# Kernel optimization log

Hardware: AMD Instinct MI355X
Metric: run time of the kernel (lower is better)

## Reference

```python
import jax, jax.numpy as jnp
import numpy as np

HIDDEN = 1024
HEADS = 16
HEAD_DIM = HIDDEN // HEADS

def setup_inputs() -> dict:
    key = jax.random.key(0)
    k1, k2, k3 = jax.random.split(key, 3)
    scale = 1.0 / np.sqrt(HIDDEN)
    return {
        "x": jax.random.normal(k1, (2, 2048, HIDDEN), dtype=jnp.float32),
        "w_qkv": jax.random.normal(k2, (HIDDEN, 3 * HIDDEN), dtype=jnp.float32) * scale,
        "b_qkv": jnp.zeros((3 * HIDDEN,), dtype=jnp.float32),
        "w_out": jax.random.normal(k3, (HIDDEN, HIDDEN), dtype=jnp.float32) * scale,
        "b_out": jnp.zeros((HIDDEN,), dtype=jnp.float32),
    }

def reference(x, w_qkv, b_qkv, w_out, b_out):
    B, S, H = x.shape
    qkv = x @ w_qkv + b_qkv                              # (B,S,3H)
    qkv = qkv.reshape(B, S, 3, HEADS, HEAD_DIM)
    qkv = jnp.transpose(qkv, (2, 0, 3, 1, 4))            # (3,B,nh,S,hd)
    q, k, v = qkv[0], qkv[1], qkv[2]
    scores = jnp.einsum("bhqd,bhkd->bhqk", q, k) / np.sqrt(HEAD_DIM)
    causal = jnp.triu(jnp.ones((S, S), dtype=bool), k=1)  # True above diagonal
    scores = jnp.where(causal, -jnp.inf, scores)
    attn = jax.nn.softmax(scores, axis=-1)               # dropout: eval mode (identity)
    out = jnp.einsum("bhqk,bhkd->bhqd", attn, v)
    out = jnp.transpose(out, (0, 2, 1, 3)).reshape(B, S, H)
    return out @ w_out + b_out
```

## Files before the change

### kernel.cpp

```cpp
#include <hip/hip_runtime.h>
#include <hip/hip_bf16.h>

typedef short short8 __attribute__((ext_vector_type(8)));
typedef short short4v __attribute__((ext_vector_type(4)));
typedef unsigned int uint4v __attribute__((ext_vector_type(4)));
typedef float f32x4 __attribute__((ext_vector_type(4)));

typedef const __attribute__((address_space(1))) unsigned int* gas_ptr;
typedef __attribute__((address_space(3))) unsigned int* las_ptr;
#define ASYNC16(g, l) __builtin_amdgcn_global_load_lds((gas_ptr)(g), (las_ptr)(l), 16, 0, 0)

__device__ __forceinline__ unsigned short f2bf(float f) {
    unsigned int u = __builtin_bit_cast(unsigned int, f);
    u += 0x7fff + ((u >> 16) & 1);
    return (unsigned short)(u >> 16);
}
__device__ __forceinline__ float bf2f(unsigned short s) {
    unsigned int u = (unsigned int)s << 16;
    return __builtin_bit_cast(float, u);
}
__device__ __forceinline__ unsigned int pkbf_trunc(float lo, float hi) {
    return __builtin_amdgcn_perm(__builtin_bit_cast(unsigned int, hi),
                                 __builtin_bit_cast(unsigned int, lo), 0x07060302u);
}

__device__ __forceinline__ void transpose_tile(
    const float* __restrict__ w, unsigned short* __restrict__ wt,
    int K, int N, int k0, int n0, unsigned short* tile)
{
    for (int i = threadIdx.x; i < 64 * 64; i += 256) {
        int r = i >> 6, c = i & 63;
        tile[r * 65 + c] = f2bf(w[(size_t)(k0 + r) * N + n0 + c]);
    }
    __syncthreads();
    for (int i = threadIdx.x; i < 64 * 64; i += 256) {
        int r = i >> 6, c = i & 63;
        wt[(size_t)(n0 + r) * K + k0 + c] = tile[c * 65 + r];
    }
}

__global__ __launch_bounds__(256) void prep(
    const float* __restrict__ x, const float* __restrict__ w_qkv,
    const float* __restrict__ w_out,
    unsigned short* __restrict__ x_b, unsigned short* __restrict__ wqkv_t,
    unsigned short* __restrict__ wout_t)
{
    __shared__ unsigned short tile[64 * 65];
    int bid = blockIdx.x;
    if (bid < 4096) {
        int i = (bid * 256 + threadIdx.x) * 4;
        float4 v = *(const float4*)(x + i);
        ushort4 o;
        o.x = f2bf(v.x); o.y = f2bf(v.y); o.z = f2bf(v.z); o.w = f2bf(v.w);
        *(ushort4*)(x_b + i) = o;
    } else if (bid < 4096 + 768) {
        int t = bid - 4096;
        transpose_tile(w_qkv, wqkv_t, 1024, 3072, (t / 48) * 64, (t % 48) * 64, tile);
    } else {
        int t = bid - 4864;
        transpose_tile(w_out, wout_t, 1024, 1024, (t >> 4) * 64, (t & 15) * 64, tile);
    }
}


template<bool OUT_BF16, bool QKV>
__global__ __launch_bounds__(256, 3) void gemm_bt(
    const unsigned short* __restrict__ A,
    const unsigned short* __restrict__ Bt,
    const float* __restrict__ bias,
    void* __restrict__ C,
    unsigned short* __restrict__ vTp,
    int M, int N, int K)
{
    __shared__ __align__(16) unsigned short As[128 * 32];
    __shared__ __align__(16) unsigned short Bs[128 * 32];
    const int tid = threadIdx.x;
    const int lane = tid & 63;
    const int wave = tid >> 6;
    const int wr = wave >> 1, wc = wave & 1;
    const int m0 = blockIdx.x * 128, n0 = blockIdx.y * 128;
    const int fr = lane & 15, fq = lane >> 4;

    f32x4 acc[4][4] = {};

    const int grow = lane >> 2;
    const int gcol = (lane & 3) * 8;
    const unsigned short* Ag = A  + (size_t)(m0 + wave * 32 + grow) * K + gcol;
    const unsigned short* Bg = Bt + (size_t)(n0 + wave * 32 + grow) * K + gcol;
    unsigned short* AsW0 = As + (wave * 32) * 32;
    unsigned short* AsW1 = As + (wave * 32 + 16) * 32;
    unsigned short* BsW0 = Bs + (wave * 32) * 32;
    unsigned short* BsW1 = Bs + (wave * 32 + 16) * 32;

    for (int k0 = 0; k0 < K; k0 += 32) {
        __syncthreads();
        ASYNC16(Ag + k0,          AsW0);
        ASYNC16(Ag + 16 * K + k0, AsW1);
        ASYNC16(Bg + k0,          BsW0);
        ASYNC16(Bg + 16 * K + k0, BsW1);
        __syncthreads();

        short8 af[4], bfr[4];
#pragma unroll
        for (int i = 0; i < 4; i++)
            af[i] = *(const short8*)(As + (wr * 64 + i * 16 + fr) * 32 + fq * 8);
#pragma unroll
        for (int j = 0; j < 4; j++)
            bfr[j] = *(const short8*)(Bs + (wc * 64 + j * 16 + fr) * 32 + fq * 8);
#pragma unroll
        for (int i = 0; i < 4; i++)
#pragma unroll
            for (int j = 0; j < 4; j++)
                acc[i][j] = __builtin_amdgcn_mfma_f32_16x16x32_bf16(af[i], bfr[j], acc[i][j], 0, 0, 0);
    }

#pragma unroll
    for (int i = 0; i < 4; i++)
#pragma unroll
        for (int j = 0; j < 4; j++) {
            int col = n0 + wc * 64 + j * 16 + fr;
            float bv = bias[col];
            if (QKV && col >= 2048) {
                int hh = (col - 2048) >> 6, d = col & 63;
#pragma unroll
                for (int r = 0; r < 4; r++) {
                    int row = m0 + wr * 64 + i * 16 + fq * 4 + r;
                    int bb = row >> 11, s = row & 2047;
                    vTp[((size_t)(bb * 16 + hh) * 64 + d) * 2048 + s] = f2bf(acc[i][j][r] + bv);
                }
            } else {
                const int cstride = QKV ? 2048 : N;
#pragma unroll
                for (int r = 0; r < 4; r++) {
                    int row = m0 + wr * 64 + i * 16 + fq * 4 + r;
                    float v = acc[i][j][r] + bv;
                    if (OUT_BF16)
                        ((unsigned short*)C)[(size_t)row * cstride + col] = f2bf(v);
                    else
                        ((float*)C)[(size_t)row * cstride + col] = v;
                }
            }
        }
}


template<int RG0>
__device__ __forceinline__ void attn_step(
    const unsigned short* __restrict__ Ks0, const unsigned short* __restrict__ Ks1,
    const unsigned short* __restrict__ Vs0, const unsigned short* __restrict__ Vs1,
    const short8 (&qf)[2][2], const short8 ones,
    f32x4 (&o_acc)[2][4], f32x4 (&l_acc)[2],
    int j0, int fr, int fq,
    const int (&qrow0)[2], bool diagA, bool diagB)
{
    short8 kf[4][2];
#pragma unroll
    for (int t = 0; t < 4; t++) {
        kf[t][0] = *(const short8*)(Ks0 + (t * 16 + fr) * 32 + fq * 8);
        kf[t][1] = *(const short8*)(Ks1 + (t * 16 + fr) * 32 + fq * 8);
    }

    short8 pf[2][2];
#pragma unroll
    for (int rg = RG0; rg < 2; rg++) {
        f32x4 s[4];
#pragma unroll
        for (int t = 0; t < 4; t++) {
            s[t] = (f32x4){0.f, 0.f, 0.f, 0.f};
            s[t] = __builtin_amdgcn_mfma_f32_16x16x32_bf16(kf[t][0], qf[rg][0], s[t], 0, 0, 0);
            s[t] = __builtin_amdgcn_mfma_f32_16x16x32_bf16(kf[t][1], qf[rg][1], s[t], 0, 0, 0);
        }
        const bool diag = rg ? diagB : diagA;
        unsigned int pk[4][2];
        if (diag) {
            const int qq = qrow0[rg] + fr;
#pragma unroll
            for (int t = 0; t < 4; t++) {
                const int keyb = j0 + t * 16 + fq * 4;
                float p[4];
#pragma unroll
                for (int r = 0; r < 4; r++) {
                    float v = __expf(s[t][r] * 0.125f - 8.0f);
                    if (keyb + r > qq) v = 0.f;
                    p[r] = v;
                }
                pk[t][0] = pkbf_trunc(p[0], p[1]);
                pk[t][1] = pkbf_trunc(p[2], p[3]);
            }
        } else {
#pragma unroll
            for (int t = 0; t < 4; t++) {
                float p[4];
#pragma unroll
                for (int r = 0; r < 4; r++)
                    p[r] = __expf(s[t][r] * 0.125f - 8.0f);
                pk[t][0] = pkbf_trunc(p[0], p[1]);
                pk[t][1] = pkbf_trunc(p[2], p[3]);
            }
        }
        pf[rg][0] = __builtin_bit_cast(short8, (uint4v){pk[0][0], pk[0][1], pk[1][0], pk[1][1]});
        pf[rg][1] = __builtin_bit_cast(short8, (uint4v){pk[2][0], pk[2][1], pk[3][0], pk[3][1]});
    }

    const int rot = (fr & 3) * 8;
    const int eo_lo = (fq * 4 - rot) & 31;
    const int eo_hi = (fq * 4 + 16 - rot) & 31;
#pragma unroll
    for (int ks = 0; ks < 2; ks++) {
        const unsigned short* Vsb = ks ? Vs1 : Vs0;
#pragma unroll
        for (int t = 0; t < 4; t++) {
            short4v vlo = *(const short4v*)(Vsb + (t * 16 + fr) * 32 + eo_lo);
            short4v vhi = *(const short4v*)(Vsb + (t * 16 + fr) * 32 + eo_hi);
            short8 vf = (short8){vlo[0], vlo[1], vlo[2], vlo[3], vhi[0], vhi[1], vhi[2], vhi[3]};
#pragma unroll
            for (int rg = RG0; rg < 2; rg++)
                o_acc[rg][t] = __builtin_amdgcn_mfma_f32_16x16x32_bf16(vf, pf[rg][ks], o_acc[rg][t], 0, 0, 0);
        }
#pragma unroll
        for (int rg = RG0; rg < 2; rg++)
            l_acc[rg] = __builtin_amdgcn_mfma_f32_16x16x32_bf16(ones, pf[rg][ks], l_acc[rg], 0, 0, 0);
    }
}

__global__ __launch_bounds__(256, 3) void flash_attn(
    const unsigned short* __restrict__ qkv,
    const unsigned short* __restrict__ vT,
    unsigned short* __restrict__ Opart,
    float* __restrict__ lpart)
{
    const int gid = blockIdx.x;
    const int bh = gid & 31;
    const int sl = gid >> 5;
    const int p  = sl & 15;
    const int g  = sl >> 4;
    const int h = bh & 15, b = bh >> 4;
    const int tid = threadIdx.x, wave = tid >> 6, lane = tid & 63;
    const int fr = lane & 15, fq = lane >> 4;
    const size_t RS = 2048;

    const unsigned short* Qb = qkv + (size_t)b * 2048 * RS + h * 64;
    const unsigned short* Kb = Qb + 1024;
    const unsigned short* Vt = vT + (size_t)(b * 16 + h) * 64 * 2048;

    __shared__ __align__(16) unsigned short Ks[2][64 * 32];
    __shared__ __align__(16) unsigned short Vs[2][64 * 32];

    short8 qf[2][2];
    int qrow0[2];
#pragma unroll
    for (int rg = 0; rg < 2; rg++) {
        int qt = rg ? (31 - p) : p;
        qrow0[rg] = qt * 64 + wave * 16;
        const unsigned short* qrow = Qb + (size_t)(qrow0[rg] + fr) * RS;
        qf[rg][0] = *(const short8*)(qrow + fq * 8);
        qf[rg][1] = *(const short8*)(qrow + 32 + fq * 8);
    }
    short8 ones;
#pragma unroll
    for (int e = 0; e < 8; e++) ones[e] = (short)0x3F80;

    f32x4 o_acc[2][4] = {};
    f32x4 l_acc[2] = {};

    const int grow = lane >> 2;
    const int gcol = (lane & 3) * 8;
    const int vrot = (grow & 3) * 8;
    const int vcol = (gcol + vrot) & 31;
    const unsigned short* Kg = Kb + (size_t)(wave * 16 + grow) * RS + gcol;
    const unsigned short* Vg = Vt + (size_t)(wave * 16 + grow) * 2048 + vcol;
    unsigned short* KsW0 = Ks[0] + (wave * 16) * 32;
    unsigned short* KsW1 = Ks[1] + (wave * 16) * 32;
    unsigned short* VsW0 = Vs[0] + (wave * 16) * 32;
    unsigned short* VsW1 = Vs[1] + (wave * 16) * 32;

    const int mid = (p >= 8) ? 8 : (16 - p);
    const int lo = g ? mid : 0;
    const int hi = g ? (32 - p) : mid;

    for (int jt = lo; jt < hi; jt++) {
        const int j0 = jt * 64;
        __syncthreads();
        ASYNC16(Kg + (size_t)j0 * RS,      KsW0);
        ASYNC16(Kg + (size_t)j0 * RS + 32, KsW1);
        ASYNC16(Vg + j0,      VsW0);
        ASYNC16(Vg + j0 + 32, VsW1);
        __syncthreads();

        bool diagA = (jt == p), diagB = (jt == 31 - p);
        if (jt <= p)
            attn_step<0>(Ks[0], Ks[1], Vs[0], Vs[1], qf, ones,
                         o_acc, l_acc, j0, fr, fq, qrow0, diagA, diagB);
        else
            attn_step<1>(Ks[0], Ks[1], Vs[0], Vs[1], qf, ones,
                         o_acc, l_acc, j0, fr, fq, qrow0, diagA, diagB);
    }

    unsigned short* Og = Opart + (size_t)g * 4096 * 1024;
    float* lg = lpart + (size_t)g * 4096 * 16;
#pragma unroll
    for (int rg = 0; rg < 2; rg++) {
        const size_t rowbase = (size_t)(b * 2048 + qrow0[rg] + fr) * 1024 + h * 64;
#pragma unroll
        for (int t = 0; t < 4; t++) {
            ushort4 o;
            o.x = f2bf(o_acc[rg][t][0]); o.y = f2bf(o_acc[rg][t][1]);
            o.z = f2bf(o_acc[rg][t][2]); o.w = f2bf(o_acc[rg][t][3]);
            *(ushort4*)(Og + rowbase + t * 16 + fq * 4) = o;
        }
        if (fq == 0)
            lg[(size_t)(b * 2048 + qrow0[rg] + fr) * 16 + h] = l_acc[rg][0];
    }
}

__global__ __launch_bounds__(256) void reduce_attn(
    const unsigned short* __restrict__ Opart, const float* __restrict__ lpart,
    unsigned short* __restrict__ out)
{
    const size_t OP = (size_t)4096 * 1024, LP = (size_t)4096 * 16;
    int i = (blockIdx.x * 256 + threadIdx.x) * 8;
    int row = i >> 10, h = (i & 1023) >> 6;
    float lsum = lpart[row * 16 + h] + lpart[LP + row * 16 + h];
    float inv = 1.0f / lsum;
    ushort4 a0 = *(const ushort4*)(Opart + i);
    ushort4 a1 = *(const ushort4*)(Opart + i + 4);
    ushort4 b0 = *(const ushort4*)(Opart + OP + i);
    ushort4 b1 = *(const ushort4*)(Opart + OP + i + 4);
    ushort4 o0, o1;
    o0.x = f2bf((bf2f(a0.x) + bf2f(b0.x)) * inv);
    o0.y = f2bf((bf2f(a0.y) + bf2f(b0.y)) * inv);
    o0.z = f2bf((bf2f(a0.z) + bf2f(b0.z)) * inv);
    o0.w = f2bf((bf2f(a0.w) + bf2f(b0.w)) * inv);
    o1.x = f2bf((bf2f(a1.x) + bf2f(b1.x)) * inv);
    o1.y = f2bf((bf2f(a1.y) + bf2f(b1.y)) * inv);
    o1.z = f2bf((bf2f(a1.z) + bf2f(b1.z)) * inv);
    o1.w = f2bf((bf2f(a1.w) + bf2f(b1.w)) * inv);
    *(ushort4*)(out + i) = o0;
    *(ushort4*)(out + i + 4) = o1;
}

extern "C" void kernel_launch(void* const* d_in, const int* in_sizes, int n_in,
                              void* d_out, int out_size, void* d_ws, size_t ws_size,
                              hipStream_t stream) {
    const float* x      = (const float*)d_in[0];
    const float* w_qkv  = (const float*)d_in[1];
    const float* b_qkv  = (const float*)d_in[2];
    const float* w_out  = (const float*)d_in[3];
    const float* b_out  = (const float*)d_in[4];
    float* out = (float*)d_out;

    char* ws = (char*)d_ws;
    const size_t MB = 1024 * 1024;
    unsigned short* qkv    = (unsigned short*)(ws);
    unsigned short* vT     = (unsigned short*)(ws + 16 * MB);
    unsigned short* wout_t = (unsigned short*)(ws + 24 * MB);
    unsigned short* attn   = (unsigned short*)(ws + 26 * MB);
    float*          lpart  = (float*)         (ws + 34 * MB);
    unsigned short* x_b    = (unsigned short*)(ws + 36 * MB);
    unsigned short* wqkv_t = (unsigned short*)(ws + 44 * MB);
    unsigned short* Opart  = (unsigned short*)(ws + 36 * MB);

    prep<<<5120, 256, 0, stream>>>(x, w_qkv, w_out, x_b, wqkv_t, wout_t);
    gemm_bt<true, true ><<<dim3(32, 24), 256, 0, stream>>>(x_b,  wqkv_t, b_qkv, qkv, vT, 4096, 3072, 1024);
    flash_attn<<<1024, 256, 0, stream>>>(qkv, vT, Opart, lpart);
    reduce_attn<<<2048, 256, 0, stream>>>(Opart, lpart, attn);
    gemm_bt<false, false><<<dim3(32, 8),  256, 0, stream>>>(attn, wout_t, b_out, out, nullptr, 4096, 1024, 1024);
}
```

Before: 194.2 us.

## Double-buffer K/V tiles in flash attention, XOR-swizzle LDS, split V transpose

The flash attention loop now double-buffers its K/V tiles in LDS. It prefetches the next tile with async global-to-LDS loads while the current one is computed, dropping one barrier per iteration. The LDS layout moves from a rotation to an XOR swizzle for both K and V reads to reduce bank conflicts. The QKV GEMM now writes V row-major into a new buffer, and a separate transpose kernel builds vT, replacing the scattered strided stores in the epilogue. The price is an extra kernel launch, an extra pass over V, and doubled LDS for flash attention, which could lower occupancy.

```diff
diff --git a/kernel.cpp b/kernel.cpp
--- a/kernel.cpp
+++ b/kernel.cpp
@@ -69,7 +69,7 @@
     const unsigned short* __restrict__ Bt,
     const float* __restrict__ bias,
     void* __restrict__ C,
-    unsigned short* __restrict__ vTp,
+    unsigned short* __restrict__ vbuf,
     int M, int N, int K)
 {
     __shared__ __align__(16) unsigned short As[128 * 32];
@@ -121,12 +121,11 @@
             int col = n0 + wc * 64 + j * 16 + fr;
             float bv = bias[col];
             if (QKV && col >= 2048) {
-                int hh = (col - 2048) >> 6, d = col & 63;
+                int cc = col - 2048;
 #pragma unroll
                 for (int r = 0; r < 4; r++) {
                     int row = m0 + wr * 64 + i * 16 + fq * 4 + r;
-                    int bb = row >> 11, s = row & 2047;
-                    vTp[((size_t)(bb * 16 + hh) * 64 + d) * 2048 + s] = f2bf(acc[i][j][r] + bv);
+                    vbuf[(size_t)row * 1024 + cc] = f2bf(acc[i][j][r] + bv);
                 }
             } else {
                 const int cstride = QKV ? 2048 : N;
@@ -143,6 +142,22 @@
         }
 }
 
+__global__ __launch_bounds__(256) void transpose_v(
+    const unsigned short* __restrict__ vbuf, unsigned short* __restrict__ vT)
+{
+    __shared__ unsigned short tile[64 * 65];
+    const int s0 = blockIdx.x * 64, h = blockIdx.y, b = blockIdx.z;
+    for (int i = threadIdx.x; i < 64 * 64; i += 256) {
+        int r = i >> 6, c = i & 63;
+        tile[r * 65 + c] = vbuf[(size_t)(b * 2048 + s0 + r) * 1024 + h * 64 + c];
+    }
+    __syncthreads();
+    for (int i = threadIdx.x; i < 64 * 64; i += 256) {
+        int r = i >> 6, c = i & 63;
+        vT[((size_t)(b * 16 + h) * 64 + r) * 2048 + s0 + c] = tile[c * 65 + r];
+    }
+}
+
 
 template<int RG0>
 __device__ __forceinline__ void attn_step(
@@ -153,11 +168,16 @@
     int j0, int fr, int fq,
     const int (&qrow0)[2], bool diagA, bool diagB)
 {
+    const int swz = (fr >> 1) & 3;
+    const int kgrp = (fq ^ swz) * 8;
+    const int voff_lo = ((((fq >> 1)    ) ^ swz) * 2 + (fq & 1)) * 4;
+    const int voff_hi = ((((fq >> 1) + 2) ^ swz) * 2 + (fq & 1)) * 4;
+
     short8 kf[4][2];
 #pragma unroll
     for (int t = 0; t < 4; t++) {
-        kf[t][0] = *(const short8*)(Ks0 + (t * 16 + fr) * 32 + fq * 8);
-        kf[t][1] = *(const short8*)(Ks1 + (t * 16 + fr) * 32 + fq * 8);
+        kf[t][0] = *(const short8*)(Ks0 + (t * 16 + fr) * 32 + kgrp);
+        kf[t][1] = *(const short8*)(Ks1 + (t * 16 + fr) * 32 + kgrp);
     }
 
     short8 pf[2][2];
@@ -202,16 +222,13 @@
         pf[rg][1] = __builtin_bit_cast(short8, (uint4v){pk[2][0], pk[2][1], pk[3][0], pk[3][1]});
     }
 
-    const int rot = (fr & 3) * 8;
-    const int eo_lo = (fq * 4 - rot) & 31;
-    const int eo_hi = (fq * 4 + 16 - rot) & 31;
 #pragma unroll
     for (int ks = 0; ks < 2; ks++) {
         const unsigned short* Vsb = ks ? Vs1 : Vs0;
 #pragma unroll
         for (int t = 0; t < 4; t++) {
-            short4v vlo = *(const short4v*)(Vsb + (t * 16 + fr) * 32 + eo_lo);
-            short4v vhi = *(const short4v*)(Vsb + (t * 16 + fr) * 32 + eo_hi);
+            short4v vlo = *(const short4v*)(Vsb + (t * 16 + fr) * 32 + voff_lo);
+            short4v vhi = *(const short4v*)(Vsb + (t * 16 + fr) * 32 + voff_hi);
             short8 vf = (short8){vlo[0], vlo[1], vlo[2], vlo[3], vhi[0], vhi[1], vhi[2], vhi[3]};
 #pragma unroll
             for (int rg = RG0; rg < 2; rg++)
@@ -243,8 +260,8 @@
     const unsigned short* Kb = Qb + 1024;
     const unsigned short* Vt = vT + (size_t)(b * 16 + h) * 64 * 2048;
 
-    __shared__ __align__(16) unsigned short Ks[2][64 * 32];
-    __shared__ __align__(16) unsigned short Vs[2][64 * 32];
+    __shared__ __align__(16) unsigned short Ks[2][2][64 * 32];
+    __shared__ __align__(16) unsigned short Vs[2][2][64 * 32];
 
     short8 qf[2][2];
     int qrow0[2];
@@ -264,35 +281,45 @@
     f32x4 l_acc[2] = {};
 
     const int grow = lane >> 2;
-    const int gcol = (lane & 3) * 8;
-    const int vrot = (grow & 3) * 8;
-    const int vcol = (gcol + vrot) & 31;
-    const unsigned short* Kg = Kb + (size_t)(wave * 16 + grow) * RS + gcol;
-    const unsigned short* Vg = Vt + (size_t)(wave * 16 + grow) * 2048 + vcol;
-    unsigned short* KsW0 = Ks[0] + (wave * 16) * 32;
-    unsigned short* KsW1 = Ks[1] + (wave * 16) * 32;
-    unsigned short* VsW0 = Vs[0] + (wave * 16) * 32;
-    unsigned short* VsW1 = Vs[1] + (wave * 16) * 32;
+    const int gcolx = (((lane & 3) ^ ((lane >> 3) & 3))) * 8;
+    const unsigned short* Kg = Kb + (size_t)(wave * 16 + grow) * RS + gcolx;
+    const unsigned short* Vg = Vt + (size_t)(wave * 16 + grow) * 2048 + gcolx;
+    unsigned short* KsW[2][2] = {
+        { Ks[0][0] + (wave * 16) * 32, Ks[0][1] + (wave * 16) * 32 },
+        { Ks[1][0] + (wave * 16) * 32, Ks[1][1] + (wave * 16) * 32 } };
+    unsigned short* VsW[2][2] = {
+        { Vs[0][0] + (wave * 16) * 32, Vs[0][1] + (wave * 16) * 32 },
+        { Vs[1][0] + (wave * 16) * 32, Vs[1][1] + (wave * 16) * 32 } };
 
     const int mid = (p >= 8) ? 8 : (16 - p);
     const int lo = g ? mid : 0;
     const int hi = g ? (32 - p) : mid;
 
+    {
+        const int j0 = lo * 64;
+        ASYNC16(Kg + (size_t)j0 * RS,      KsW[0][0]);
+        ASYNC16(Kg + (size_t)j0 * RS + 32, KsW[0][1]);
+        ASYNC16(Vg + j0,      VsW[0][0]);
+        ASYNC16(Vg + j0 + 32, VsW[0][1]);
+    }
+
     for (int jt = lo; jt < hi; jt++) {
+        const int buf = (jt - lo) & 1;
+        __syncthreads();
+        if (jt + 1 < hi) {
+            const int jn = (jt + 1) * 64;
+            ASYNC16(Kg + (size_t)jn * RS,      KsW[buf ^ 1][0]);
+            ASYNC16(Kg + (size_t)jn * RS + 32, KsW[buf ^ 1][1]);
+            ASYNC16(Vg + jn,      VsW[buf ^ 1][0]);
+            ASYNC16(Vg + jn + 32, VsW[buf ^ 1][1]);
+        }
         const int j0 = jt * 64;
-        __syncthreads();
-        ASYNC16(Kg + (size_t)j0 * RS,      KsW0);
-        ASYNC16(Kg + (size_t)j0 * RS + 32, KsW1);
-        ASYNC16(Vg + j0,      VsW0);
-        ASYNC16(Vg + j0 + 32, VsW1);
-        __syncthreads();
-
         bool diagA = (jt == p), diagB = (jt == 31 - p);
         if (jt <= p)
-            attn_step<0>(Ks[0], Ks[1], Vs[0], Vs[1], qf, ones,
+            attn_step<0>(Ks[buf][0], Ks[buf][1], Vs[buf][0], Vs[buf][1], qf, ones,
                          o_acc, l_acc, j0, fr, fq, qrow0, diagA, diagB);
         else
-            attn_step<1>(Ks[0], Ks[1], Vs[0], Vs[1], qf, ones,
+            attn_step<1>(Ks[buf][0], Ks[buf][1], Vs[buf][0], Vs[buf][1], qf, ones,
                          o_acc, l_acc, j0, fr, fq, qrow0, diagA, diagB);
     }
 
@@ -359,9 +386,11 @@
     unsigned short* x_b    = (unsigned short*)(ws + 36 * MB);
     unsigned short* wqkv_t = (unsigned short*)(ws + 44 * MB);
     unsigned short* Opart  = (unsigned short*)(ws + 36 * MB);
+    unsigned short* vbuf   = (unsigned short*)(ws + 52 * MB);
 
     prep<<<5120, 256, 0, stream>>>(x, w_qkv, w_out, x_b, wqkv_t, wout_t);
-    gemm_bt<true, true ><<<dim3(32, 24), 256, 0, stream>>>(x_b,  wqkv_t, b_qkv, qkv, vT, 4096, 3072, 1024);
+    gemm_bt<true, true ><<<dim3(32, 24), 256, 0, stream>>>(x_b,  wqkv_t, b_qkv, qkv, vbuf, 4096, 3072, 1024);
+    transpose_v<<<dim3(32, 16, 2), 256, 0, stream>>>(vbuf, vT);
     flash_attn<<<1024, 256, 0, stream>>>(qkv, vT, Opart, lpart);
     reduce_attn<<<2048, 256, 0, stream>>>(Opart, lpart, attn);
     gemm_bt<false, false><<<dim3(32, 8),  256, 0, stream>>>(attn, wout_t, b_out, out, nullptr, 4096, 1024, 1024);
```

New measurement: 194.7 us. No clear change (+0.2%).
